# Performance work log

Measured on AMD Instinct MI355X. Metric: run time of the kernel, lower is better.

The kernel has to match this reference:

```python
import jax, jax.numpy as jnp
import numpy as np
from math import pi as PI

N = 50000      # nodes
E = 800000     # edges
G = 512        # graphs
L = 6          # num_layers
D = 128        # hidden_channels
F = 128        # num_filters
NG = 50        # num_gaussians
IN = 28        # input_dim
OUT = 32       # out_channels
CUT = 6.0      # cutoff
LN2 = float(np.log(2.0))
BN_EPS = 1e-5


def ssp(x):
    # ShiftedSoftplus
    return jax.nn.softplus(x) - LN2


def setup_inputs() -> dict:
    key = jax.random.key(0)
    ks = jax.random.split(key, 16)
    def rn(i, shape, s=0.05):
        return jax.random.normal(ks[i], shape, dtype=jnp.float32) * s
    return {
        "x": jax.random.normal(ks[0], (N, IN), dtype=jnp.float32),
        "pos": jax.random.normal(ks[1], (N, 3), dtype=jnp.float32) * 3.0,
        "batch": jnp.sort(jax.random.randint(ks[2], (N,), 0, G)),
        "edge_index": jax.random.randint(ks[3], (2, E), 0, N),
        # FeatureEmbedding: Linear(28,64) -> BN(64) -> ReLU -> Linear(64,128) -> ReLU
        "fe_w1": rn(4, (IN, D // 2)), "fe_b1": jnp.zeros((D // 2,), jnp.float32),
        "bn_gamma": jnp.ones((D // 2,), jnp.float32), "bn_beta": jnp.zeros((D // 2,), jnp.float32),
        "fe_w2": rn(5, (D // 2, D)), "fe_b2": jnp.zeros((D,), jnp.float32),
        # per-layer update_e: lin (no bias), mlp: Linear(NG,F)->SSP->Linear(F,F)
        "lin_w": rn(6, (L, D, F)),
        "mlp_w1": rn(7, (L, NG, F)), "mlp_b1": jnp.zeros((L, F), jnp.float32),
        "mlp_w2": rn(8, (L, F, F)), "mlp_b2": jnp.zeros((L, F), jnp.float32),
        # per-layer update_v: Linear(F,D)->SSP->Linear(D,D), residual
        "v1_w": rn(9, (L, F, D)), "v1_b": jnp.zeros((L, D), jnp.float32),
        "v2_w": rn(10, (L, D, D)), "v2_b": jnp.zeros((L, D), jnp.float32),
        # update_u: Linear(D,D//2)->SSP->Linear(D//2,OUT), then scatter over graphs
        "u1_w": rn(11, (D, D // 2)), "u1_b": jnp.zeros((D // 2,), jnp.float32),
        "u2_w": rn(12, (D // 2, OUT)), "u2_b": jnp.zeros((OUT,), jnp.float32),
    }


def reference(x, pos, batch, edge_index,
              fe_w1, fe_b1, bn_gamma, bn_beta, fe_w2, fe_b2,
              lin_w, mlp_w1, mlp_b1, mlp_w2, mlp_b2,
              v1_w, v1_b, v2_w, v2_b,
              u1_w, u1_b, u2_w, u2_b):
    row, col = edge_index[0], edge_index[1]  # (j, i): gather source j, scatter target i
    d = pos[row] - pos[col]                  # [E,3]
    dist = jnp.sqrt(jnp.sum(d * d, axis=-1))  # [E]
    offset = jnp.linspace(0.0, CUT, NG)
    coeff = -0.5 / (offset[1] - offset[0]) ** 2
    dist_emb = jnp.exp(coeff * (dist[:, None] - offset[None, :]) ** 2)  # [E,NG]
    cosC = 0.5 * (jnp.cos(dist * PI / CUT) + 1.0)                        # [E]

    # FeatureEmbedding (BatchNorm in training mode: batch statistics)
    h = x @ fe_w1 + fe_b1
    mu = jnp.mean(h, axis=0)
    var = jnp.mean((h - mu) ** 2, axis=0)
    h = (h - mu) / jnp.sqrt(var + BN_EPS) * bn_gamma + bn_beta
    h = jax.nn.relu(h)
    v = jax.nn.relu(h @ fe_w2 + fe_b2)  # [N,D]

    for l in range(L):
        # update_e: gate MLP on gaussian embedding, cosine cutoff, gather v[j]
        W = (ssp(dist_emb @ mlp_w1[l] + mlp_b1[l]) @ mlp_w2[l] + mlp_b2[l]) * cosC[:, None]  # [E,F]
        e = (v @ lin_w[l])[row] * W                                                          # [E,F]
        # update_v: scatter-add to nodes, MLP, residual
        agg = jax.ops.segment_sum(e, col, num_segments=N)                                    # [N,F]
        v = v + (ssp(agg @ v1_w[l] + v1_b[l]) @ v2_w[l] + v2_b[l])

    # update_u: per-node MLP then scatter-add per graph
    s = ssp(v @ u1_w + u1_b) @ u2_w + u2_b  # [N,OUT]
    return jax.ops.segment_sum(s, batch, num_segments=G)  # [G,OUT]
```

## Files before the change

### kernel.cpp

```cpp
#include <hip/hip_runtime.h>
#include <hip/hip_fp16.h>
#include <math.h>

#define DEV __device__ __forceinline__

constexpr int NGAUSS = 50;
constexpr int LAY = 6;
constexpr int K_TAB = 8192;
constexpr float DMAX = 40.0f;
constexpr float TSCALE = (float)(K_TAB - 1) / DMAX;
constexpr float STEP = 6.0f / 49.0f;
constexpr float COEFF = -0.5f / (STEP * STEP);
constexpr float LN2F = 0.69314718055994531f;
constexpr float PI_OVER_CUT = 0.52359877559829887f;

using f16x8 = __attribute__((ext_vector_type(8))) _Float16;
using f16x4 = __attribute__((ext_vector_type(4))) _Float16;
using f32x4 = __attribute__((ext_vector_type(4))) float;

#define MFMA16(a, b, c) __builtin_amdgcn_mfma_f32_16x16x32_f16(a, b, c, 0, 0, 0)

DEV float sspf(float x) {
    float ax = fabsf(x);
    float e = __expf(-ax);
    return fmaxf(x, 0.f) + __logf(1.f + e) - LN2F;
}

DEV float4 ld_h4(const ushort* p) {
    uint2 r = *(const uint2*)p;
    __half2 a = __builtin_bit_cast(__half2, r.x);
    __half2 b = __builtin_bit_cast(__half2, r.y);
    float2 fa = __half22float2(a), fb = __half22float2(b);
    return make_float4(fa.x, fa.y, fb.x, fb.y);
}
DEV void st_h4(ushort* p, float4 v) {
    uint2 r;
    r.x = __builtin_bit_cast(uint, __float22half2_rn(make_float2(v.x, v.y)));
    r.y = __builtin_bit_cast(uint, __float22half2_rn(make_float2(v.z, v.w)));
    *(uint2*)p = r;
}

__global__ void k_cvtT128(const float* __restrict__ src, ushort* __restrict__ dst) {
    const float* s = src + (size_t)blockIdx.x * 16384;
    ushort* d = dst + (size_t)blockIdx.x * 16384;
    for (int i = threadIdx.x; i < 16384; i += 256) {
        int k = i >> 7, c = i & 127;
        d[(c << 7) + k] = __builtin_bit_cast(ushort, (_Float16)s[i]);
    }
}
__global__ void k_cvtT_fe(const float* __restrict__ src, ushort* __restrict__ dst) {
    for (int i = threadIdx.x; i < 8192; i += 256) {
        int k = i >> 7, c = i & 127;
        dst[(c << 6) + k] = __builtin_bit_cast(ushort, (_Float16)src[i]);
    }
}

__global__ void k_hist(const int* __restrict__ ei, int* __restrict__ counts, int E) {
    int e = blockIdx.x * 256 + threadIdx.x;
    if (e < E) atomicAdd(&counts[ei[E + e]], 1);
}

__global__ void k_scan1(const int* __restrict__ counts, int* __restrict__ locex,
                        int* __restrict__ bsum, int n) {
    __shared__ int s_wsum[16];
    const int tid = threadIdx.x;
    const int i = blockIdx.x * 1024 + tid;
    const int lane = tid & 63, wv = tid >> 6;
    int v = (i < n) ? counts[i] : 0;
    int x = v;
    #pragma unroll
    for (int off = 1; off < 64; off <<= 1) {
        int y = __shfl_up(x, off, 64);
        if (lane >= off) x += y;
    }
    if (lane == 63) s_wsum[wv] = x;
    __syncthreads();
    if (wv == 0 && lane < 16) {
        int wval = s_wsum[lane];
        int wx = wval;
        #pragma unroll
        for (int off = 1; off < 16; off <<= 1) {
            int wy = __shfl_up(wx, off, 16);
            if (lane >= off) wx += wy;
        }
        s_wsum[lane] = wx - wval;
    }
    __syncthreads();
    if (i < n) locex[i] = s_wsum[wv] + x - v;
    if (tid == 1023) bsum[blockIdx.x] = s_wsum[15] + x;
}

__global__ void k_scan2(int* __restrict__ bsum, int nb) {
    __shared__ int s_wsum[16];
    const int tid = threadIdx.x;
    const int lane = tid & 63, wv = tid >> 6;
    int v = (tid < nb) ? bsum[tid] : 0;
    int x = v;
    #pragma unroll
    for (int off = 1; off < 64; off <<= 1) {
        int y = __shfl_up(x, off, 64);
        if (lane >= off) x += y;
    }
    if (lane == 63) s_wsum[wv] = x;
    __syncthreads();
    if (wv == 0 && lane < 16) {
        int wval = s_wsum[lane];
        int wx = wval;
        #pragma unroll
        for (int off = 1; off < 16; off <<= 1) {
            int wy = __shfl_up(wx, off, 16);
            if (lane >= off) wx += wy;
        }
        s_wsum[lane] = wx - wval;
    }
    __syncthreads();
    if (tid < nb) bsum[tid] = s_wsum[wv] + x - v;
}

__global__ void k_scan3(const int* __restrict__ locex, const int* __restrict__ bsumex,
                        int* __restrict__ cursor, int* __restrict__ rowptr, int n) {
    int i = blockIdx.x * 256 + threadIdx.x;
    if (i >= n) return;
    int e = locex[i] + bsumex[i >> 10];
    cursor[i] = e;
    rowptr[i] = e;
}

__global__ void k_scatter(const int* __restrict__ ei, const float* __restrict__ pos,
                          int* __restrict__ cursor, uint2* __restrict__ s_ef, int E) {
    int e = blockIdx.x * 256 + threadIdx.x;
    if (e >= E) return;
    int r = ei[e], c = ei[E + e];
    int p = atomicAdd(&cursor[c], 1);
    float dx = pos[3 * r + 0] - pos[3 * c + 0];
    float dy = pos[3 * r + 1] - pos[3 * c + 1];
    float dz = pos[3 * r + 2] - pos[3 * c + 2];
    float d = sqrtf(dx * dx + dy * dy + dz * dz);
    float fid = fminf(d * TSCALE, (float)(K_TAB - 2) + 0.999f);
    s_ef[p] = make_uint2((uint)r, __builtin_bit_cast(uint, fid));
}

__launch_bounds__(256)
__global__ void k_tab_all(const float* __restrict__ w1A, const float* __restrict__ b1A,
                          const float* __restrict__ w2A, const float* __restrict__ b2A,
                          ushort* __restrict__ tabA) {
    const int layer = blockIdx.x >> 8;
    const int k0 = (blockIdx.x & 255) * 32;
    const float* w1 = w1A + (size_t)layer * NGAUSS * 128;
    const float* b1 = b1A + (size_t)layer * 128;
    const float* w2 = w2A + (size_t)layer * 128 * 128;
    const float* b2 = b2A + (size_t)layer * 128;
    ushort* tab = tabA + (size_t)layer * K_TAB * 128;

    __shared__ float s_demb[32][NGAUSS];
    __shared__ float s_t1[32][128];
    const int tid = threadIdx.x;

    for (int i = tid; i < 32 * NGAUSS; i += 256) {
        int r = i / NGAUSS, g = i - r * NGAUSS;
        float d = (float)(k0 + r) * (1.0f / TSCALE);
        float t = d - g * STEP;
        s_demb[r][g] = __expf(COEFF * t * t);
    }
    __syncthreads();

    const int cg = tid & 31, rg = tid >> 5;
    const int r0 = rg << 2;
    const int c4 = cg << 2;

    float4 b1v = *(const float4*)&b1[c4];
    float4 acc[4];
    #pragma unroll
    for (int i = 0; i < 4; i++) acc[i] = b1v;
    #pragma unroll 2
    for (int k = 0; k < NGAUSS; k++) {
        float4 wv = *(const float4*)&w1[(k << 7) + c4];
        #pragma unroll
        for (int i = 0; i < 4; i++) {
            float dv = s_demb[r0 + i][k];
            acc[i].x = fmaf(dv, wv.x, acc[i].x);
            acc[i].y = fmaf(dv, wv.y, acc[i].y);
            acc[i].z = fmaf(dv, wv.z, acc[i].z);
            acc[i].w = fmaf(dv, wv.w, acc[i].w);
        }
    }
    #pragma unroll
    for (int i = 0; i < 4; i++) {
        float4 t;
        t.x = sspf(acc[i].x); t.y = sspf(acc[i].y);
        t.z = sspf(acc[i].z); t.w = sspf(acc[i].w);
        *(float4*)&s_t1[r0 + i][c4] = t;
    }
    __syncthreads();

    float4 b2v = *(const float4*)&b2[c4];
    float4 a2[4];
    #pragma unroll
    for (int i = 0; i < 4; i++) a2[i] = b2v;
    #pragma unroll 4
    for (int k = 0; k < 128; k++) {
        float4 wv = *(const float4*)&w2[(k << 7) + c4];
        #pragma unroll
        for (int i = 0; i < 4; i++) {
            float tv = s_t1[r0 + i][k];
            a2[i].x = fmaf(tv, wv.x, a2[i].x);
            a2[i].y = fmaf(tv, wv.y, a2[i].y);
            a2[i].z = fmaf(tv, wv.z, a2[i].z);
            a2[i].w = fmaf(tv, wv.w, a2[i].w);
        }
    }
    #pragma unroll
    for (int i = 0; i < 4; i++) {
        int knot = k0 + r0 + i;
        float d = (float)knot * (1.0f / TSCALE);
        float cc = 0.5f * (__cosf(d * PI_OVER_CUT) + 1.0f);
        float4 o;
        o.x = a2[i].x * cc; o.y = a2[i].y * cc;
        o.z = a2[i].z * cc; o.w = a2[i].w * cc;
        st_h4(&tab[((size_t)knot << 7) + c4], o);
    }
}

__global__ void k_pair(const ushort* __restrict__ tab, ushort* __restrict__ tab2) {
    size_t idx = (size_t)blockIdx.x * 256 + threadIdx.x;
    int cg = idx & 31;
    size_t knotg = idx >> 5;
    int knot = (int)(knotg & (K_TAB - 1));
    const ushort* r0 = tab + (knotg << 7) + (cg << 2);
    const ushort* r1 = (knot < K_TAB - 1) ? r0 + 128 : r0;
    uint2 a = *(const uint2*)r0;
    uint2 b = *(const uint2*)r1;
    ushort4 al = *(const ushort4*)&a;
    ushort4 bl = *(const ushort4*)&b;
    ushort out[8] = {al.x, bl.x, al.y, bl.y, al.z, bl.z, al.w, bl.w};
    *(uint4*)&tab2[(knotg << 8) + (cg << 3)] = *(const uint4*)out;
}

__launch_bounds__(256, 8)
__global__ void k_edge_csr(const uint2* __restrict__ s_ef,
                           const int* __restrict__ rowptr, const int* __restrict__ counts,
                           const ushort* __restrict__ vlin, const ushort* __restrict__ tab2,
                           ushort* __restrict__ agg, int N) {
    const int tid = threadIdx.x;
    const int cg = tid & 31;
    const int n = blockIdx.x * 8 + (tid >> 5);
    if (n >= N) return;
    const ushort* tabc = tab2 + (cg << 3);
    const ushort* vlc = vlin + (cg << 2);

    const int rs = rowptr[n];
    const int re = rs + counts[n];
    float4 run = make_float4(0.f, 0.f, 0.f, 0.f);
    int e = rs;
    for (; e + 8 <= re; e += 8) {
        f16x8 TP[8];
        f16x4 VL[8];
        _Float16 FR[8];
        #pragma unroll
        for (int j = 0; j < 8; j++) {
            uint2 ef = s_ef[e + j];
            float fid = __builtin_bit_cast(float, ef.y);
            int i0 = (int)fid;
            FR[j] = (_Float16)(fid - (float)i0);
            TP[j] = *(const f16x8*)(tabc + ((size_t)i0 << 8));
            VL[j] = *(const f16x4*)(vlc + ((size_t)ef.x << 7));
        }
        f16x4 p0 = {0, 0, 0, 0}, p1 = {0, 0, 0, 0};
        #pragma unroll
        for (int j = 0; j < 8; j += 2) {
            f16x4 t0a = {TP[j][0], TP[j][2], TP[j][4], TP[j][6]};
            f16x4 t1a = {TP[j][1], TP[j][3], TP[j][5], TP[j][7]};
            f16x4 t0b = {TP[j+1][0], TP[j+1][2], TP[j+1][4], TP[j+1][6]};
            f16x4 t1b = {TP[j+1][1], TP[j+1][3], TP[j+1][5], TP[j+1][7]};
            f16x4 w0 = t0a + FR[j]     * (t1a - t0a);
            f16x4 w1 = t0b + FR[j + 1] * (t1b - t0b);
            p0 += w0 * VL[j];
            p1 += w1 * VL[j + 1];
        }
        run.x += (float)p0[0] + (float)p1[0];
        run.y += (float)p0[1] + (float)p1[1];
        run.z += (float)p0[2] + (float)p1[2];
        run.w += (float)p0[3] + (float)p1[3];
    }
    for (; e < re; e++) {
        uint2 ef = s_ef[e];
        float fid = __builtin_bit_cast(float, ef.y);
        int i0 = (int)fid;
        _Float16 fr = (_Float16)(fid - (float)i0);
        f16x8 tp = *(const f16x8*)(tabc + ((size_t)i0 << 8));
        f16x4 vl = *(const f16x4*)(vlc + ((size_t)ef.x << 7));
        f16x4 t0 = {tp[0], tp[2], tp[4], tp[6]};
        f16x4 t1 = {tp[1], tp[3], tp[5], tp[7]};
        f16x4 w = t0 + fr * (t1 - t0);
        f16x4 p = w * vl;
        run.x += (float)p[0];
        run.y += (float)p[1];
        run.z += (float)p[2];
        run.w += (float)p[3];
    }
    st_h4(&agg[((size_t)n << 7) + (cg << 2)], run);
}

__global__ void k_fe1(const float* __restrict__ x, const float* __restrict__ w,
                      const float* __restrict__ b, float* __restrict__ h, int N) {
    int idx = blockIdx.x * 256 + threadIdx.x;
    if (idx >= N * 64) return;
    int n = idx >> 6, c = idx & 63;
    const float* xr = x + (size_t)n * 28;
    float acc = b[c];
    #pragma unroll
    for (int k = 0; k < 28; k++) acc = fmaf(xr[k], w[k * 64 + c], acc);
    h[idx] = acc;
}

__global__ void k_bnstat(const float* __restrict__ h, float* __restrict__ stats, int N) {
    __shared__ float s_s[256], s_q[256];
    int tid = threadIdx.x;
    int c = tid & 63, g = tid >> 6;
    float s = 0.f, q = 0.f;
    for (int n = blockIdx.x * 4 + g; n < N; n += gridDim.x * 4) {
        float v = h[(size_t)n * 64 + c];
        s += v; q += v * v;
    }
    s_s[tid] = s; s_q[tid] = q;
    __syncthreads();
    if (tid < 64) {
        s = s_s[tid] + s_s[tid + 64] + s_s[tid + 128] + s_s[tid + 192];
        q = s_q[tid] + s_q[tid + 64] + s_q[tid + 128] + s_q[tid + 192];
        atomicAdd(&stats[tid], s);
        atomicAdd(&stats[64 + tid], q);
    }
}

__global__ void k_bnfin(const float* __restrict__ stats, float* __restrict__ prm,
                        const float* __restrict__ gamma, const float* __restrict__ beta,
                        float invN) {
    int c = threadIdx.x;
    float mu = stats[c] * invN;
    float var = stats[64 + c] * invN - mu * mu;
    float sc = gamma[c] * rsqrtf(var + 1e-5f);
    prm[c] = sc;
    prm[64 + c] = beta[c] - mu * sc;
}

__launch_bounds__(256, 4)
__global__ void k_fe2(const float* __restrict__ h, const float* __restrict__ prm,
                      const ushort* __restrict__ w2T, const float* __restrict__ b2,
                      ushort* __restrict__ v16, int N) {
    constexpr int LDP = 72;
    __shared__ _Float16 sH[64 * LDP];
    const int tid = threadIdx.x;
    const int n0 = blockIdx.x * 64;

    for (int i = tid; i < 64 * 16; i += 256) {
        int row = i >> 4, c4 = (i & 15) << 2;
        int gr = n0 + row;
        float4 hv = (gr < N) ? *(const float4*)&h[((size_t)gr << 6) + c4]
                             : make_float4(0.f, 0.f, 0.f, 0.f);
        float4 sc = *(const float4*)&prm[c4];
        float4 sh = *(const float4*)&prm[64 + c4];
        f16x4 o;
        o[0] = (_Float16)fmaxf(fmaf(hv.x, sc.x, sh.x), 0.f);
        o[1] = (_Float16)fmaxf(fmaf(hv.y, sc.y, sh.y), 0.f);
        o[2] = (_Float16)fmaxf(fmaf(hv.z, sc.z, sh.z), 0.f);
        o[3] = (_Float16)fmaxf(fmaf(hv.w, sc.w, sh.w), 0.f);
        *(f16x4*)&sH[row * LDP + c4] = o;
    }
    __syncthreads();

    const int wid = tid >> 6, lane = tid & 63;
    const int lr = lane & 15, lg = lane >> 4;
    const int kof = lg << 3;
    const int arow = wid * 16 + lr;
    const int drow0 = wid * 16 + (lg << 2);

    f16x8 a0 = *(const f16x8*)&sH[arow * LDP + kof];
    f16x8 a1 = *(const f16x8*)&sH[arow * LDP + 32 + kof];

    #pragma unroll
    for (int n = 0; n < 8; n++) {
        const ushort* bp = w2T + (((size_t)(n << 4) + lr) << 6);
        f32x4 c = {0.f, 0.f, 0.f, 0.f};
        c = MFMA16(a0, *(const f16x8*)(bp + kof), c);
        c = MFMA16(a1, *(const f16x8*)(bp + 32 + kof), c);
        int col = (n << 4) + lr;
        float bb = b2[col];
        #pragma unroll
        for (int r = 0; r < 4; r++) {
            int gr = n0 + drow0 + r;
            if (gr < N) v16[((size_t)gr << 7) + col] =
                __builtin_bit_cast(ushort, (_Float16)fmaxf(c[r] + bb, 0.f));
        }
    }
}

__launch_bounds__(256, 4)
__global__ void k_gemm_rb(const ushort* __restrict__ A, const ushort* __restrict__ wT,
                          ushort* __restrict__ C, int N) {
    constexpr int LDP = 136;
    __shared__ _Float16 sA[64 * LDP];
    const int tid = threadIdx.x;
    const int n0 = blockIdx.x * 64;

    for (int i = tid; i < 64 * 32; i += 256) {
        int row = i >> 5, c4 = (i & 31) << 2;
        int gr = n0 + row;
        uint2 val = (gr < N) ? *(const uint2*)&A[((size_t)gr << 7) + c4]
                             : make_uint2(0u, 0u);
        *(uint2*)&sA[row * LDP + c4] = val;
    }
    __syncthreads();

    const int wid = tid >> 6, lane = tid & 63;
    const int lr = lane & 15, lg = lane >> 4;
    const int kof = lg << 3;
    const int arow = wid * 16 + lr;
    const int drow0 = wid * 16 + (lg << 2);

    f16x8 a0 = *(const f16x8*)&sA[arow * LDP + kof];
    f16x8 a1 = *(const f16x8*)&sA[arow * LDP + 32 + kof];
    f16x8 a2 = *(const f16x8*)&sA[arow * LDP + 64 + kof];
    f16x8 a3 = *(const f16x8*)&sA[arow * LDP + 96 + kof];

    #pragma unroll
    for (int n = 0; n < 8; n++) {
        const ushort* bp = wT + (((size_t)(n << 4) + lr) << 7);
        f32x4 c = {0.f, 0.f, 0.f, 0.f};
        c = MFMA16(a0, *(const f16x8*)(bp + kof), c);
        c = MFMA16(a1, *(const f16x8*)(bp + 32 + kof), c);
        c = MFMA16(a2, *(const f16x8*)(bp + 64 + kof), c);
        c = MFMA16(a3, *(const f16x8*)(bp + 96 + kof), c);
        int col = (n << 4) + lr;
        #pragma unroll
        for (int r = 0; r < 4; r++) {
            int gr = n0 + drow0 + r;
            if (gr < N) C[((size_t)gr << 7) + col] =
                __builtin_bit_cast(ushort, (_Float16)c[r]);
        }
    }
}

__launch_bounds__(512, 8)
__global__ void k_update(const ushort* __restrict__ agg,
                         const ushort* __restrict__ w1T, const float* __restrict__ b1,
                         const ushort* __restrict__ w2T, const float* __restrict__ b2,
                         ushort* __restrict__ v16,
                         const ushort* __restrict__ linT, ushort* __restrict__ vlin, int N) {
    constexpr int LDP = 136;
    __shared__ _Float16 sA[64 * LDP];
    __shared__ _Float16 sB[64 * LDP];
    const int tid = threadIdx.x;
    const int n0 = blockIdx.x * 64;

    for (int i = tid; i < 64 * 32; i += 512) {
        int row = i >> 5, c4 = (i & 31) << 2;
        int gr = n0 + row;
        uint2 a = (gr < N) ? *(const uint2*)&agg[((size_t)gr << 7) + c4] : make_uint2(0u, 0u);
        uint2 b = (gr < N) ? *(const uint2*)&v16[((size_t)gr << 7) + c4] : make_uint2(0u, 0u);
        *(uint2*)&sA[row * LDP + c4] = a;
        *(uint2*)&sB[row * LDP + c4] = b;
    }
    __syncthreads();

    const int wid = tid >> 6, lane = tid & 63;
    const int lr = lane & 15, lg = lane >> 4;
    const int kof = lg << 3;
    const int col = (wid << 4) + lr;
    const int dr0 = lg << 2;

    f32x4 acc[4];

    {
        const ushort* bp = w1T + ((size_t)col << 7);
        f16x8 B0 = *(const f16x8*)(bp + kof);
        f16x8 B1 = *(const f16x8*)(bp + 32 + kof);
        f16x8 B2 = *(const f16x8*)(bp + 64 + kof);
        f16x8 B3 = *(const f16x8*)(bp + 96 + kof);
        #pragma unroll
        for (int rb = 0; rb < 4; rb++) {
            const _Float16* ap = &sA[((rb << 4) + lr) * LDP + kof];
            f32x4 c = {0.f, 0.f, 0.f, 0.f};
            c = MFMA16(*(const f16x8*)ap, B0, c);
            c = MFMA16(*(const f16x8*)(ap + 32), B1, c);
            c = MFMA16(*(const f16x8*)(ap + 64), B2, c);
            c = MFMA16(*(const f16x8*)(ap + 96), B3, c);
            acc[rb] = c;
        }
    }
    __syncthreads();
    {
        float bb = b1[col];
        #pragma unroll
        for (int rb = 0; rb < 4; rb++) {
            #pragma unroll
            for (int r = 0; r < 4; r++)
                sA[((rb << 4) + dr0 + r) * LDP + col] = (_Float16)sspf(acc[rb][r] + bb);
        }
    }
    __syncthreads();

    {
        const ushort* bp = w2T + ((size_t)col << 7);
        f16x8 B0 = *(const f16x8*)(bp + kof);
        f16x8 B1 = *(const f16x8*)(bp + 32 + kof);
        f16x8 B2 = *(const f16x8*)(bp + 64 + kof);
        f16x8 B3 = *(const f16x8*)(bp + 96 + kof);
        #pragma unroll
        for (int rb = 0; rb < 4; rb++) {
            const _Float16* ap = &sA[((rb << 4) + lr) * LDP + kof];
            f32x4 c = {0.f, 0.f, 0.f, 0.f};
            c = MFMA16(*(const f16x8*)ap, B0, c);
            c = MFMA16(*(const f16x8*)(ap + 32), B1, c);
            c = MFMA16(*(const f16x8*)(ap + 64), B2, c);
            c = MFMA16(*(const f16x8*)(ap + 96), B3, c);
            acc[rb] = c;
        }
    }
    {
        float bb = b2[col];
        #pragma unroll
        for (int rb = 0; rb < 4; rb++) {
            #pragma unroll
            for (int r = 0; r < 4; r++) {
                _Float16* p = &sB[((rb << 4) + dr0 + r) * LDP + col];
                *p = (_Float16)(acc[rb][r] + bb + (float)*p);
            }
        }
    }
    __syncthreads();

    for (int i = tid; i < 64 * 32; i += 512) {
        int row = i >> 5, c4 = (i & 31) << 2;
        int gr = n0 + row;
        if (gr < N) *(uint2*)&v16[((size_t)gr << 7) + c4] = *(const uint2*)&sB[row * LDP + c4];
    }
    if (!linT) return;

    {
        const ushort* bp = linT + ((size_t)col << 7);
        f16x8 B0 = *(const f16x8*)(bp + kof);
        f16x8 B1 = *(const f16x8*)(bp + 32 + kof);
        f16x8 B2 = *(const f16x8*)(bp + 64 + kof);
        f16x8 B3 = *(const f16x8*)(bp + 96 + kof);
        #pragma unroll
        for (int rb = 0; rb < 4; rb++) {
            const _Float16* ap = &sB[((rb << 4) + lr) * LDP + kof];
            f32x4 c = {0.f, 0.f, 0.f, 0.f};
            c = MFMA16(*(const f16x8*)ap, B0, c);
            c = MFMA16(*(const f16x8*)(ap + 32), B1, c);
            c = MFMA16(*(const f16x8*)(ap + 64), B2, c);
            c = MFMA16(*(const f16x8*)(ap + 96), B3, c);
            acc[rb] = c;
        }
    }
    #pragma unroll
    for (int rb = 0; rb < 4; rb++) {
        #pragma unroll
        for (int r = 0; r < 4; r++)
            sA[((rb << 4) + dr0 + r) * LDP + col] = (_Float16)acc[rb][r];
    }
    __syncthreads();

    for (int i = tid; i < 64 * 32; i += 512) {
        int row = i >> 5, c4 = (i & 31) << 2;
        int gr = n0 + row;
        if (gr < N) *(uint2*)&vlin[((size_t)gr << 7) + c4] = *(const uint2*)&sA[row * LDP + c4];
    }
}

__launch_bounds__(256, 4)
__global__ void k_uout(const ushort* __restrict__ v16, const float* __restrict__ u1w,
                       const float* __restrict__ u1b, const float* __restrict__ u2w,
                       const float* __restrict__ u2b, const int* __restrict__ batch,
                       float* __restrict__ out, int N) {
    __shared__ float sA[64 * 128];
    const int tid = threadIdx.x;
    const int n0 = blockIdx.x * 64;

    for (int i = tid; i < 64 * 32; i += 256) {
        int row = i >> 5, cq = (i & 31) << 2;
        int gr = n0 + row;
        float4 val = make_float4(0.f, 0.f, 0.f, 0.f);
        if (gr < N) val = ld_h4(&v16[((size_t)gr << 7) + cq]);
        *(float4*)&sA[row * 128 + cq] = val;
    }
    __syncthreads();

    const int cg = tid & 31, rg = tid >> 5;
    const int r0 = rg << 3;
    const int c2 = cg << 1;

    float2 acc[8];
    {
        float2 b1v = *(const float2*)&u1b[c2];
        #pragma unroll
        for (int i = 0; i < 8; i++) acc[i] = b1v;
        #pragma unroll 4
        for (int k = 0; k < 128; k++) {
            float2 wv = *(const float2*)&u1w[(k << 6) + c2];
            #pragma unroll
            for (int i = 0; i < 8; i++) {
                float a = sA[(r0 + i) * 128 + k];
                acc[i].x = fmaf(a, wv.x, acc[i].x);
                acc[i].y = fmaf(a, wv.y, acc[i].y);
            }
        }
    }
    __syncthreads();
    #pragma unroll
    for (int i = 0; i < 8; i++) {
        sA[(r0 + i) * 64 + c2 + 0] = sspf(acc[i].x);
        sA[(r0 + i) * 64 + c2 + 1] = sspf(acc[i].y);
    }
    __syncthreads();

    float acc2[8];
    {
        float bb = u2b[cg];
        #pragma unroll
        for (int i = 0; i < 8; i++) acc2[i] = bb;
        #pragma unroll 4
        for (int k = 0; k < 64; k++) {
            float wv = u2w[(k << 5) + cg];
            #pragma unroll
            for (int i = 0; i < 8; i++)
                acc2[i] = fmaf(sA[(r0 + i) * 64 + k], wv, acc2[i]);
        }
    }

    int cur = -1;
    float run = 0.f;
    #pragma unroll
    for (int i = 0; i < 8; i++) {
        int gr = n0 + r0 + i;
        int g = (gr < N) ? batch[gr] : -1;
        if (g != cur) {
            if (cur >= 0) atomicAdd(&out[(size_t)cur * 32 + cg], run);
            cur = g;
            run = 0.f;
        }
        if (g >= 0) run += acc2[i];
    }
    if (cur >= 0) atomicAdd(&out[(size_t)cur * 32 + cg], run);
}

extern "C" void kernel_launch(void* const* d_in, const int* in_sizes, int n_in,
                              void* d_out, int out_size, void* d_ws, size_t ws_size,
                              hipStream_t stream) {
    const float* x      = (const float*)d_in[0];
    const float* pos    = (const float*)d_in[1];
    const int*   batch  = (const int*)d_in[2];
    const int*   ei     = (const int*)d_in[3];
    const float* fe_w1  = (const float*)d_in[4];
    const float* fe_b1  = (const float*)d_in[5];
    const float* bn_g   = (const float*)d_in[6];
    const float* bn_b   = (const float*)d_in[7];
    const float* fe_w2  = (const float*)d_in[8];
    const float* fe_b2  = (const float*)d_in[9];
    const float* lin_w  = (const float*)d_in[10];
    const float* mlp_w1 = (const float*)d_in[11];
    const float* mlp_b1 = (const float*)d_in[12];
    const float* mlp_w2 = (const float*)d_in[13];
    const float* mlp_b2 = (const float*)d_in[14];
    const float* v1_w   = (const float*)d_in[15];
    const float* v1_b   = (const float*)d_in[16];
    const float* v2_w   = (const float*)d_in[17];
    const float* v2_b   = (const float*)d_in[18];
    const float* u1_w   = (const float*)d_in[19];
    const float* u1_b   = (const float*)d_in[20];
    const float* u2_w   = (const float*)d_in[21];
    const float* u2_b   = (const float*)d_in[22];

    const int N = in_sizes[0] / 28;
    const int E = in_sizes[3] / 2;
    const int NB1 = (N + 1023) / 1024;

    char* ws = (char*)d_ws;
    size_t o = 0;
    auto alloc = [&](size_t bytes) { void* p = ws + o; o += (bytes + 255) & ~(size_t)255; return p; };
    int*    counts = (int*)   alloc((size_t)N * 4);
    int*    cursor = (int*)   alloc((size_t)N * 4);
    int*    rowptr = (int*)   alloc((size_t)N * 4);
    int*    bsum   = (int*)   alloc((size_t)NB1 * 4);
    uint2*  s_ef   = (uint2*) alloc((size_t)E * 8);
    float*  stats  = (float*) alloc(128 * 4);
    float*  prm    = (float*) alloc(128 * 4);
    ushort* tab    = (ushort*)alloc((size_t)LAY * K_TAB * 128 * 2);
    ushort* tab2   = (ushort*)alloc((size_t)LAY * K_TAB * 256 * 2);
    ushort* v16    = (ushort*)alloc((size_t)N * 128 * 2);
    ushort* vlin   = (ushort*)alloc((size_t)N * 128 * 2);
    ushort* agg    = (ushort*)alloc((size_t)N * 128 * 2);
    float*  h      = (float*) alloc((size_t)N * 64 * 4);
    int*    locex  = (int*)   alloc((size_t)N * 4);
    ushort* v1T    = (ushort*)alloc((size_t)LAY * 16384 * 2);
    ushort* v2T    = (ushort*)alloc((size_t)LAY * 16384 * 2);
    ushort* linT   = (ushort*)alloc((size_t)LAY * 16384 * 2);
    ushort* fe2T   = (ushort*)alloc((size_t)8192 * 2);

    k_cvtT128<<<LAY, 256, 0, stream>>>(v1_w, v1T);
    k_cvtT128<<<LAY, 256, 0, stream>>>(v2_w, v2T);
    k_cvtT128<<<LAY, 256, 0, stream>>>(lin_w, linT);
    k_cvtT_fe<<<1, 256, 0, stream>>>(fe_w2, fe2T);

    hipMemsetAsync(counts, 0, (size_t)N * 4, stream);
    k_hist<<<(E + 255) / 256, 256, 0, stream>>>(ei, counts, E);
    k_scan1<<<NB1, 1024, 0, stream>>>(counts, locex, bsum, N);
    k_scan2<<<1, 1024, 0, stream>>>(bsum, NB1);
    k_scan3<<<(N + 255) / 256, 256, 0, stream>>>(locex, bsum, cursor, rowptr, N);
    k_scatter<<<(E + 255) / 256, 256, 0, stream>>>(ei, pos, cursor, s_ef, E);

    k_tab_all<<<LAY * 256, 256, 0, stream>>>(mlp_w1, mlp_b1, mlp_w2, mlp_b2, tab);
    k_pair<<<LAY * K_TAB * 32 / 256, 256, 0, stream>>>(tab, tab2);

    hipMemsetAsync(stats, 0, 128 * 4, stream);
    k_fe1<<<(N * 64 + 255) / 256, 256, 0, stream>>>(x, fe_w1, fe_b1, h, N);
    k_bnstat<<<256, 256, 0, stream>>>(h, stats, N);
    k_bnfin<<<1, 64, 0, stream>>>(stats, prm, bn_g, bn_b, 1.0f / (float)N);
    const int gblk = (N + 63) / 64;
    k_fe2<<<gblk, 256, 0, stream>>>(h, prm, fe2T, fe_b2, v16, N);

    k_gemm_rb<<<gblk, 256, 0, stream>>>(v16, linT, vlin, N);

    const int eblk = (N + 7) / 8;
    for (int l = 0; l < LAY; l++) {
        k_edge_csr<<<eblk, 256, 0, stream>>>(
            s_ef, rowptr, counts, vlin,
            tab2 + (size_t)l * K_TAB * 256, agg, N);
        const ushort* lin_next = (l + 1 < LAY) ? linT + (size_t)(l + 1) * 16384 : nullptr;
        k_update<<<gblk, 512, 0, stream>>>(
            agg, v1T + (size_t)l * 16384, v1_b + (size_t)l * 128,
            v2T + (size_t)l * 16384, v2_b + (size_t)l * 128,
            v16, lin_next, vlin, N);
    }

    hipMemsetAsync(d_out, 0, (size_t)out_size * 4, stream);
    k_uout<<<gblk, 256, 0, stream>>>(v16, u1_w, u1_b, u2_w, u2_b, batch, (float*)d_out, N);
}
```

Measured before the change: 721.7 us.

## Replace interpolated gate table with nearest-knot lookup and packed edge records

```diff
diff --git a/kernel.cpp b/kernel.cpp
--- a/kernel.cpp
+++ b/kernel.cpp
@@ -6,7 +6,7 @@
 
 constexpr int NGAUSS = 50;
 constexpr int LAY = 6;
-constexpr int K_TAB = 8192;
+constexpr int K_TAB = 16384;
 constexpr float DMAX = 40.0f;
 constexpr float TSCALE = (float)(K_TAB - 1) / DMAX;
 constexpr float STEP = 6.0f / 49.0f;
@@ -17,6 +17,7 @@
 using f16x8 = __attribute__((ext_vector_type(8))) _Float16;
 using f16x4 = __attribute__((ext_vector_type(4))) _Float16;
 using f32x4 = __attribute__((ext_vector_type(4))) float;
+using f32x8 = __attribute__((ext_vector_type(8))) float;
 
 #define MFMA16(a, b, c) __builtin_amdgcn_mfma_f32_16x16x32_f16(a, b, c, 0, 0, 0)
 
@@ -127,7 +128,7 @@
 }
 
 __global__ void k_scatter(const int* __restrict__ ei, const float* __restrict__ pos,
-                          int* __restrict__ cursor, uint2* __restrict__ s_ef, int E) {
+                          int* __restrict__ cursor, uint* __restrict__ s_ef, int E) {
     int e = blockIdx.x * 256 + threadIdx.x;
     if (e >= E) return;
     int r = ei[e], c = ei[E + e];
@@ -136,16 +137,17 @@
     float dy = pos[3 * r + 1] - pos[3 * c + 1];
     float dz = pos[3 * r + 2] - pos[3 * c + 2];
     float d = sqrtf(dx * dx + dy * dy + dz * dz);
-    float fid = fminf(d * TSCALE, (float)(K_TAB - 2) + 0.999f);
-    s_ef[p] = make_uint2((uint)r, __builtin_bit_cast(uint, fid));
+    int i0 = (int)(d * TSCALE + 0.5f);
+    if (i0 > K_TAB - 1) i0 = K_TAB - 1;
+    s_ef[p] = (uint)r | ((uint)i0 << 16);
 }
 
 __launch_bounds__(256)
 __global__ void k_tab_all(const float* __restrict__ w1A, const float* __restrict__ b1A,
                           const float* __restrict__ w2A, const float* __restrict__ b2A,
                           ushort* __restrict__ tabA) {
-    const int layer = blockIdx.x >> 8;
-    const int k0 = (blockIdx.x & 255) * 32;
+    const int layer = blockIdx.x / (K_TAB / 32);
+    const int k0 = (blockIdx.x % (K_TAB / 32)) * 32;
     const float* w1 = w1A + (size_t)layer * NGAUSS * 128;
     const float* b1 = b1A + (size_t)layer * 128;
     const float* w2 = w2A + (size_t)layer * 128 * 128;
@@ -221,84 +223,54 @@
     }
 }
 
-__global__ void k_pair(const ushort* __restrict__ tab, ushort* __restrict__ tab2) {
-    size_t idx = (size_t)blockIdx.x * 256 + threadIdx.x;
-    int cg = idx & 31;
-    size_t knotg = idx >> 5;
-    int knot = (int)(knotg & (K_TAB - 1));
-    const ushort* r0 = tab + (knotg << 7) + (cg << 2);
-    const ushort* r1 = (knot < K_TAB - 1) ? r0 + 128 : r0;
-    uint2 a = *(const uint2*)r0;
-    uint2 b = *(const uint2*)r1;
-    ushort4 al = *(const ushort4*)&a;
-    ushort4 bl = *(const ushort4*)&b;
-    ushort out[8] = {al.x, bl.x, al.y, bl.y, al.z, bl.z, al.w, bl.w};
-    *(uint4*)&tab2[(knotg << 8) + (cg << 3)] = *(const uint4*)out;
-}
-
 __launch_bounds__(256, 8)
-__global__ void k_edge_csr(const uint2* __restrict__ s_ef,
+__global__ void k_edge_csr(const uint* __restrict__ s_ef,
                            const int* __restrict__ rowptr, const int* __restrict__ counts,
-                           const ushort* __restrict__ vlin, const ushort* __restrict__ tab2,
+                           const ushort* __restrict__ vlin, const ushort* __restrict__ tab,
                            ushort* __restrict__ agg, int N) {
     const int tid = threadIdx.x;
-    const int cg = tid & 31;
+    const int l32 = tid & 31;
+    const int h = l32 >> 4;
+    const int lc = l32 & 15;
     const int n = blockIdx.x * 8 + (tid >> 5);
     if (n >= N) return;
-    const ushort* tabc = tab2 + (cg << 3);
-    const ushort* vlc = vlin + (cg << 2);
+    const ushort* tabc = tab + (lc << 3);
+    const ushort* vlc  = vlin + (lc << 3);
 
     const int rs = rowptr[n];
     const int re = rs + counts[n];
-    float4 run = make_float4(0.f, 0.f, 0.f, 0.f);
-    int e = rs;
-    for (; e + 8 <= re; e += 8) {
-        f16x8 TP[8];
-        f16x4 VL[8];
-        _Float16 FR[8];
-        #pragma unroll
-        for (int j = 0; j < 8; j++) {
-            uint2 ef = s_ef[e + j];
-            float fid = __builtin_bit_cast(float, ef.y);
-            int i0 = (int)fid;
-            FR[j] = (_Float16)(fid - (float)i0);
-            TP[j] = *(const f16x8*)(tabc + ((size_t)i0 << 8));
-            VL[j] = *(const f16x4*)(vlc + ((size_t)ef.x << 7));
-        }
-        f16x4 p0 = {0, 0, 0, 0}, p1 = {0, 0, 0, 0};
-        #pragma unroll
-        for (int j = 0; j < 8; j += 2) {
-            f16x4 t0a = {TP[j][0], TP[j][2], TP[j][4], TP[j][6]};
-            f16x4 t1a = {TP[j][1], TP[j][3], TP[j][5], TP[j][7]};
-            f16x4 t0b = {TP[j+1][0], TP[j+1][2], TP[j+1][4], TP[j+1][6]};
-            f16x4 t1b = {TP[j+1][1], TP[j+1][3], TP[j+1][5], TP[j+1][7]};
-            f16x4 w0 = t0a + FR[j]     * (t1a - t0a);
-            f16x4 w1 = t0b + FR[j + 1] * (t1b - t0b);
-            p0 += w0 * VL[j];
-            p1 += w1 * VL[j + 1];
-        }
-        run.x += (float)p0[0] + (float)p1[0];
-        run.y += (float)p0[1] + (float)p1[1];
-        run.z += (float)p0[2] + (float)p1[2];
-        run.w += (float)p0[3] + (float)p1[3];
-    }
-    for (; e < re; e++) {
-        uint2 ef = s_ef[e];
-        float fid = __builtin_bit_cast(float, ef.y);
-        int i0 = (int)fid;
-        _Float16 fr = (_Float16)(fid - (float)i0);
-        f16x8 tp = *(const f16x8*)(tabc + ((size_t)i0 << 8));
-        f16x4 vl = *(const f16x4*)(vlc + ((size_t)ef.x << 7));
-        f16x4 t0 = {tp[0], tp[2], tp[4], tp[6]};
-        f16x4 t1 = {tp[1], tp[3], tp[5], tp[7]};
-        f16x4 w = t0 + fr * (t1 - t0);
-        f16x4 p = w * vl;
-        run.x += (float)p[0];
-        run.y += (float)p[1];
-        run.z += (float)p[2];
-        run.w += (float)p[3];
-    }
-    st_h4(&agg[((size_t)n << 7) + (cg << 2)], run);
+    f32x8 acc = {0.f, 0.f, 0.f, 0.f, 0.f, 0.f, 0.f, 0.f};
+
+    int e = rs + h;
+    for (; e + 6 < re; e += 8) {
+        f16x8 TP[4], VL[4];
+        #pragma unroll
+        for (int j = 0; j < 4; j++) {
+            uint pk = s_ef[e + 2 * j];
+            TP[j] = *(const f16x8*)(tabc + ((size_t)(pk >> 16) << 7));
+            VL[j] = *(const f16x8*)(vlc + ((size_t)(pk & 0xFFFFu) << 7));
+        }
+        f16x8 p0 = TP[0] * VL[0];
+        p0 += TP[1] * VL[1];
+        f16x8 p1 = TP[2] * VL[2];
+        p1 += TP[3] * VL[3];
+        acc += __builtin_convertvector(p0, f32x8);
+        acc += __builtin_convertvector(p1, f32x8);
+    }
+    for (; e < re; e += 2) {
+        uint pk = s_ef[e];
+        f16x8 tp = *(const f16x8*)(tabc + ((size_t)(pk >> 16) << 7));
+        f16x8 vl = *(const f16x8*)(vlc + ((size_t)(pk & 0xFFFFu) << 7));
+        acc += __builtin_convertvector(tp * vl, f32x8);
+    }
+    #pragma unroll
+    for (int i = 0; i < 8; i++) acc[i] += __shfl_xor(acc[i], 16);
+    if (h == 0) {
+        f16x8 o;
+        #pragma unroll
+        for (int i = 0; i < 8; i++) o[i] = (_Float16)acc[i];
+        *(f16x8*)&agg[((size_t)n << 7) + (lc << 3)] = o;
+    }
 }
 
 __global__ void k_fe1(const float* __restrict__ x, const float* __restrict__ w,
@@ -682,11 +654,10 @@
     int*    cursor = (int*)   alloc((size_t)N * 4);
     int*    rowptr = (int*)   alloc((size_t)N * 4);
     int*    bsum   = (int*)   alloc((size_t)NB1 * 4);
-    uint2*  s_ef   = (uint2*) alloc((size_t)E * 8);
+    uint*   s_ef   = (uint*)  alloc((size_t)E * 4);
     float*  stats  = (float*) alloc(128 * 4);
     float*  prm    = (float*) alloc(128 * 4);
     ushort* tab    = (ushort*)alloc((size_t)LAY * K_TAB * 128 * 2);
-    ushort* tab2   = (ushort*)alloc((size_t)LAY * K_TAB * 256 * 2);
     ushort* v16    = (ushort*)alloc((size_t)N * 128 * 2);
     ushort* vlin   = (ushort*)alloc((size_t)N * 128 * 2);
     ushort* agg    = (ushort*)alloc((size_t)N * 128 * 2);
@@ -709,8 +680,7 @@
     k_scan3<<<(N + 255) / 256, 256, 0, stream>>>(locex, bsum, cursor, rowptr, N);
     k_scatter<<<(E + 255) / 256, 256, 0, stream>>>(ei, pos, cursor, s_ef, E);
 
-    k_tab_all<<<LAY * 256, 256, 0, stream>>>(mlp_w1, mlp_b1, mlp_w2, mlp_b2, tab);
-    k_pair<<<LAY * K_TAB * 32 / 256, 256, 0, stream>>>(tab, tab2);
+    k_tab_all<<<LAY * (K_TAB / 32), 256, 0, stream>>>(mlp_w1, mlp_b1, mlp_w2, mlp_b2, tab);
 
     hipMemsetAsync(stats, 0, 128 * 4, stream);
     k_fe1<<<(N * 64 + 255) / 256, 256, 0, stream>>>(x, fe_w1, fe_b1, h, N);
@@ -725,7 +695,7 @@
     for (int l = 0; l < LAY; l++) {
         k_edge_csr<<<eblk, 256, 0, stream>>>(
             s_ef, rowptr, counts, vlin,
-            tab2 + (size_t)l * K_TAB * 256, agg, N);
+            tab + (size_t)l * K_TAB * 128, agg, N);
         const ushort* lin_next = (l + 1 < LAY) ? linT + (size_t)(l + 1) * 16384 : nullptr;
         k_update<<<gblk, 512, 0, stream>>>(
             agg, v1T + (size_t)l * 16384, v1_b + (size_t)l * 128,
```

Result: faster. 654.3 us (-9.3%).
